# Kernel optimization log

Measured on AMD Instinct MI355X. Metric: run time of the kernel, lower is better.

Reference implementation:

```python
import jax, jax.numpy as jnp
import numpy as np

J = 1.0        # adhesion coupling
TEMP = 1.0     # Metropolis temperature
MCS_STEPS = 4  # monte-carlo sweeps per forward
N_CELL_TYPES = 16


def setup_inputs() -> dict:
    key = jax.random.key(0)
    k1, k2, k3, k4 = jax.random.split(key, 4)
    B, C, H, W = 8, 8, 1024, 1024
    X = jax.random.normal(k1, (B, C, H, W), dtype=jnp.float32)
    # channel 0 is the cell-ID image: small non-negative integer labels
    ids = jax.random.randint(k2, (B, H, W), 0, N_CELL_TYPES).astype(jnp.float32)
    X = X.at[:, 0].set(ids)
    conv_w = jax.random.normal(k3, (4, C), dtype=jnp.float32) * 0.1  # 1x1 conv: C -> 4
    conv_b = jax.random.normal(k4, (4,), dtype=jnp.float32) * 0.1
    return {"X": X, "conv_w": conv_w, "conv_b": conv_b}


def _neighbors(ids):
    # (B,H,W) -> (B,H,W,4): up, down, left, right via periodic roll
    return jnp.stack([
        jnp.roll(ids, (-1, 0), (-2, -1)),
        jnp.roll(ids, (1, 0), (-2, -1)),
        jnp.roll(ids, (0, -1), (-2, -1)),
        jnp.roll(ids, (0, 1), (-2, -1)),
    ], axis=-1)


def _cpm_forward(X, conv_w, conv_b):
    B, C, H, W = X.shape
    # 1x1 conv producing per-direction NN energy term dH_NN: (B,H,W,4)
    dH_NN = jnp.einsum('bchw,oc->bhwo', X, conv_w) + conv_b
    ids = X[:, 0]
    yy = jnp.arange(H)[:, None]
    xx = jnp.arange(W)[None, :]
    parity = ((yy + xx) % 2).astype(jnp.int32)  # checkerboard decomposition

    keys = jax.random.split(jax.random.key(42), 2 * MCS_STEPS)
    subs = jnp.tile(jnp.array([0, 1], jnp.int32), MCS_STEPS)

    def half_step(ids, carry):
        k, sub = carry
        k1, k2 = jax.random.split(k)
        dirs = jax.random.randint(k1, (B, H, W), 0, 4)            # random flip-source direction
        nb = _neighbors(ids)                                       # (B,H,W,4)
        src = jnp.take_along_axis(nb, dirs[..., None], -1)[..., 0]
        # local adhesion dH: J * (unlike-neighbor count after flip - before)
        dH_adh = J * (jnp.sum(nb != src[..., None], -1)
                      - jnp.sum(nb != ids[..., None], -1)).astype(ids.dtype)
        dH_nn = jnp.take_along_axis(dH_NN, dirs[..., None], -1)[..., 0]
        dH = dH_adh + dH_nn
        u = jax.random.uniform(k2, (B, H, W))
        accept = (u < jnp.exp(-dH / TEMP)) & (parity == sub)
        return jnp.where(accept, src, ids), None

    ids, _ = jax.lax.scan(half_step, ids, (keys, subs))
    return X.at[:, 0].set(ids)


def reference(X, conv_w, conv_b):
    return _cpm_forward(X, conv_w, conv_b)
```

## Files before the change

### kernel.cpp

```cpp
#include <hip/hip_runtime.h>
#include <stdint.h>


#define HW    1048576
#define BHWu  8388608u
#define NHu   4194304u

struct KeysK { uint32_t d[8][2]; uint32_t u[8][2]; };

__device__ __host__ __forceinline__ void tf2x32(uint32_t k0, uint32_t k1,
                                                uint32_t x0, uint32_t x1,
                                                uint32_t& o0, uint32_t& o1) {
  uint32_t k2 = k0 ^ k1 ^ 0x1BD11BDAu;
  x0 += k0; x1 += k1;
#define RDD(r) { x0 += x1; x1 = (x1 << (r)) | (x1 >> (32 - (r))); x1 ^= x0; }
  RDD(13) RDD(15) RDD(26) RDD(6)
  x0 += k1; x1 += k2 + 1u;
  RDD(17) RDD(29) RDD(16) RDD(24)
  x0 += k2; x1 += k0 + 2u;
  RDD(13) RDD(15) RDD(26) RDD(6)
  x0 += k0; x1 += k1 + 3u;
  RDD(17) RDD(29) RDD(16) RDD(24)
  x0 += k1; x1 += k2 + 4u;
  RDD(13) RDD(15) RDD(26) RDD(6)
  x0 += k2; x1 += k0 + 5u;
#undef RDD
  o0 = x0; o1 = x1;
}

__device__ __forceinline__ float xla_expf(float input) {
  float x  = fmaxf(fminf(input, 88.3762626647950f), -88.3762626647949f);
  float fx = floorf(fmaf(x, 1.44269504088896341f, 0.5f));
  float tmp = __fmul_rn(0.693359375f, fx);
  float z   = __fmul_rn(-2.12194440e-4f, fx);
  x = __fsub_rn(x, tmp);
  x = __fsub_rn(x, z);
  z = __fmul_rn(x, x);
  float y = fmaf(x, 1.9875691500e-4f, 1.3981999507e-3f);
  y = fmaf(y, x, 8.3334519073e-3f);
  y = fmaf(y, x, 4.1665795894e-2f);
  y = fmaf(y, x, 1.6666665459e-1f);
  y = fmaf(y, x, 5.0000001201e-1f);
  y = fmaf(y, z, x);
  y = __fadd_rn(y, 1.0f);
  int n = (int)fx;
  float p2n = __int_as_float((n + 127) << 23);
  return fmaxf(__fmul_rn(y, p2n), input);
}

#define BY(v, i) ((uint32_t)(((v) >> ((i) * 8)) & 0xffu))
#define ACC_D(dd) (u < xla_expf(-__fadd_rn((float)(dd), v)))

__global__ __launch_bounds__(256) void prep_fused4(const float* __restrict__ X,
                                                   const float* __restrict__ W,
                                                   const float* __restrict__ Bb,
                                                   uint8_t* __restrict__ code,
                                                   uint8_t* __restrict__ ids,
                                                   float* __restrict__ out,
                                                   KeysK K) {
  const uint32_t tid = threadIdx.x;
  const uint32_t g = blockIdx.x, group = g / 23u, r = g - group * 23u;
  if (r >= 16u) {
    uint32_t j = group * 7u + (r - 16u);
    const float4* X4 = (const float4*)X;
    float4*       O4 = (float4*)out;
#pragma unroll
    for (uint32_t i = 0; i < 16u; i++) {
      uint32_t F = j * 4096u + i * 256u + tid;
      uint32_t b = F / 1835008u;
      uint32_t rem = F - b * 1835008u;
      size_t idx = ((size_t)b << 21) + 262144u + rem;
      O4[idx] = X4[idx];
    }
    return;
  }
  const uint32_t row = group * 16u + r;
  const uint32_t b = row >> 10, y = row & 1023u;
  const uint32_t ylsb = y & 1u;
  const uint32_t x0 = 4u * tid;

  const float4* xb = (const float4*)(X + ((size_t)b << 23));
  const uint32_t fq = (y << 8) + tid;

  float acc[4][4];
  float c0[4];
#pragma unroll
  for (int c = 0; c < 8; c++) {
    float4 a = xb[((uint32_t)c << 18) + fq];
    float xs[4] = {a.x, a.y, a.z, a.w};
    if (c == 0) {
#pragma unroll
      for (int px = 0; px < 4; px++) c0[px] = xs[px];
    }
#pragma unroll
    for (int px = 0; px < 4; px++)
#pragma unroll
      for (int o = 0; o < 4; o++) {
        float m = __fmul_rn(xs[px], W[o * 8 + c]);
        acc[px][o] = (c == 0) ? __fadd_rn(0.0f, m) : __fadd_rn(acc[px][o], m);
      }
  }
#pragma unroll
  for (int px = 0; px < 4; px++)
#pragma unroll
    for (int o = 0; o < 4; o++) acc[px][o] = __fadd_rn(acc[px][o], Bb[o]);

  {
    uchar4 v;
    v.x = (uint8_t)(int)c0[0]; v.y = (uint8_t)(int)c0[1];
    v.z = (uint8_t)(int)c0[2]; v.w = (uint8_t)(int)c0[3];
    *(uchar4*)(ids + (b << 20) + (y << 10) + x0) = v;
  }

  const uint32_t pbase   = (b << 20) | (y << 10);
  const uint32_t codeoff = (b << 19) | (y << 9) | (x0 >> 1);
#pragma unroll
  for (int js = 0; js < 4; js++) {
#pragma unroll
    for (int pb = 0; pb < 2; pb++) {
      uint32_t s0 = ylsb ^ (uint32_t)pb;
      uint32_t dka = s0 ? K.d[2 * js + 1][0] : K.d[2 * js][0];
      uint32_t dkb = s0 ? K.d[2 * js + 1][1] : K.d[2 * js][1];
      uint32_t uka = s0 ? K.u[2 * js + 1][0] : K.u[2 * js][0];
      uint32_t ukb = s0 ? K.u[2 * js + 1][1] : K.u[2 * js][1];
      uint32_t cword = 0;
#pragma unroll
      for (int k = 0; k < 2; k++) {
        int px = 2 * k + pb;
        uint32_t p = pbase | (x0 + (uint32_t)px);
        uint32_t o0, o1, q0, q1;
        tf2x32(dka, dkb, 0u, p, o0, o1);
        uint32_t dir = (o0 ^ o1) & 3u;
        tf2x32(uka, ukb, 0u, p, q0, q1);
        uint32_t ub = (q0 ^ q1) >> 9;
        float u = __fsub_rn(__uint_as_float(ub | 0x3F800000u), 1.0f);
        float v = (dir == 0) ? acc[px][0] : (dir == 1) ? acc[px][1]
                : (dir == 2) ? acc[px][2] : acc[px][3];
        int dstar;
        if (ub == 0u) {
          dstar = 4;
        } else {
          float l2  = __log2f(u);
          float tau = fmaf(-0.693147180559945f, l2, -v);
          float gf  = floorf(tau);
          float fr  = tau - gf;
          int   gi  = (int)fmaxf(fminf(gf, 6.0f), -7.0f);
          dstar = gi;
          if (fr < 1e-4f)        dstar = ACC_D(gi)     ? gi     : gi - 1;
          else if (fr > 0.9999f) dstar = ACC_D(gi + 1) ? gi + 1 : gi;
        }
        dstar = dstar < -5 ? -5 : (dstar > 4 ? 4 : dstar);
        cword |= (uint32_t)((uint32_t)(dstar + 5) | (dir << 4)) << (8 * k);
      }
      uint32_t t = 2u * (uint32_t)js + s0;
      *(uint16_t*)(code + (size_t)t * NHu + codeoff) = (uint16_t)cword;
    }
  }
}

template <int LAST>
__global__ __launch_bounds__(256) void step_d(uint8_t* __restrict__ ids,
                                              const uint8_t* __restrict__ codeT,
                                              float* __restrict__ out,
                                              int subi) {
  uint32_t n   = blockIdx.x * 256u + (uint32_t)threadIdx.x;
  uint32_t sub = (uint32_t)subi;
  uint32_t b   = n >> 17;
  uint32_t y   = (n >> 7) & 1023u;
  uint32_t c   = (y + sub) & 1u;
  uint32_t X8  = (n & 127u) << 3;
  uint32_t rowp = (b << 20) | (y << 10);
  uint32_t upp  = (b << 20) | (((y + 1u) & 1023u) << 10);
  uint32_t dnp  = (b << 20) | (((y - 1u) & 1023u) << 10);

  uint32_t cw = *(const uint32_t*)(codeT + ((b << 19) | (y << 9) | ((n & 127u) << 2)));

  uint64_t mid = *(const uint64_t*)(ids + rowp + X8);
  uint64_t up  = *(const uint64_t*)(ids + upp + X8);
  uint64_t dn  = *(const uint64_t*)(ids + dnp + X8);
  uint32_t e   = c ? (uint32_t)ids[rowp + ((X8 + 8u) & 1023u)]
                   : (uint32_t)ids[rowp + ((X8 + 1023u) & 1023u)];

  uint32_t nw[4];
#pragma unroll
  for (int k = 0; k < 4; k++) {
    uint32_t self  = c ? BY(mid, 2 * k + 1) : BY(mid, 2 * k);
    uint32_t left  = c ? BY(mid, 2 * k)
                       : ((k == 0) ? e : BY(mid, 2 * k - 1));
    uint32_t right = c ? ((k == 3) ? e : BY(mid, 2 * k + 2))
                       : BY(mid, 2 * k + 1);
    uint32_t n0 = c ? BY(up, 2 * k + 1) : BY(up, 2 * k);
    uint32_t n1 = c ? BY(dn, 2 * k + 1) : BY(dn, 2 * k);

    uint32_t bk  = (cw >> (8 * k)) & 0xffu;
    uint32_t dir = (bk >> 4) & 3u;
    uint32_t ds5 = bk & 15u;
    uint32_t s  = (dir == 0) ? n0 : (dir == 1) ? n1 : (dir == 2) ? right : left;
    int dadh = ((int)(n0 != s) + (int)(n1 != s) + (int)(right != s) + (int)(left != s))
             - ((int)(n0 != self) + (int)(n1 != self) + (int)(right != self) + (int)(left != self));
    nw[k] = ((uint32_t)(dadh + 5) <= ds5) ? s : self;
  }

  if (!LAST) {
    uint64_t A = (uint64_t)nw[0] | ((uint64_t)nw[1] << 16)
               | ((uint64_t)nw[2] << 32) | ((uint64_t)nw[3] << 48);
    uint64_t mask = 0x00FF00FF00FF00FFull << (8u * c);
    uint64_t nm = (mid & ~mask) | (A << (8u * c));
    *(uint64_t*)(ids + rowp + X8) = nm;
  } else {
    float f[8];
#pragma unroll
    for (int j = 0; j < 8; j++) {
      uint32_t bj = (((uint32_t)j & 1u) == c) ? nw[j >> 1] : BY(mid, j);
      f[j] = (float)bj;
    }
    float4 f0 = {f[0], f[1], f[2], f[3]};
    float4 f1 = {f[4], f[5], f[6], f[7]};
    float* op = out + ((size_t)b << 23) + (y << 10) + X8;
    *(float4*)op       = f0;
    *(float4*)(op + 4) = f1;
  }
}

__device__ __forceinline__ void metro_one(uint32_t u, uint32_t sub,
                                          uint8_t* __restrict__ ids,
                                          const float* __restrict__ dHNN,
                                          uint32_t dk0, uint32_t dk1,
                                          uint32_t uk0, uint32_t uk1) {
  uint32_t b = u >> 19;
  uint32_t r = u & 524287u;
  uint32_t y = r >> 9;
  uint32_t i = r & 511u;
  uint32_t x = (i << 1) | ((y + sub) & 1u);
  uint32_t p = (b << 20) | (y << 10) | x;
  float4 dnn = ((const float4*)dHNN)[sub * NHu + u];
  uint32_t d0, d1, u0, u1;
  tf2x32(dk0, dk1, 0u, p, d0, d1);
  uint32_t db = d0 ^ d1;
  tf2x32(uk0, uk1, 0u, p, u0, u1);
  uint32_t ub = u0 ^ u1;
  int   dir = (int)(db & 3u);
  float uu  = __fsub_rn(__uint_as_float((ub >> 9) | 0x3F800000u), 1.0f);
  uint32_t yN = (y + 1) & 1023u, yP = (y - 1) & 1023u;
  uint32_t xN = (x + 1) & 1023u, xP = (x - 1) & 1023u;
  uint32_t base = b << 20;
  uint32_t cc = ids[p];
  uint32_t n0 = ids[base + (yN << 10) + x];
  uint32_t n1 = ids[base + (yP << 10) + x];
  uint32_t n2 = ids[base + (y << 10) + xN];
  uint32_t n3 = ids[base + (y << 10) + xP];
  uint32_t s  = (dir == 0) ? n0 : (dir == 1) ? n1 : (dir == 2) ? n2 : n3;
  float dH_nn = (dir == 0) ? dnn.x : (dir == 1) ? dnn.y : (dir == 2) ? dnn.z : dnn.w;
  int dadh = ((int)(n0 != s) + (int)(n1 != s) + (int)(n2 != s) + (int)(n3 != s))
           - ((int)(n0 != cc) + (int)(n1 != cc) + (int)(n2 != cc) + (int)(n3 != cc));
  float dH = __fadd_rn((float)dadh, dH_nn);
  if (uu < xla_expf(-dH)) ids[p] = (uint8_t)s;
}

__global__ __launch_bounds__(256) void prep4_fb(const float* __restrict__ X,
                                                const float* __restrict__ W,
                                                const float* __restrict__ Bb,
                                                float* __restrict__ dHNN,
                                                uint8_t* __restrict__ ids) {
  int tid = blockIdx.x * 256 + threadIdx.x;
  int e   = tid << 2;
  int b   = e >> 20;
  int yx  = e & (HW - 1);
  int y   = yx >> 10;
  int x0  = yx & 1023;
  int q4  = yx >> 2;
  const float4* xb = (const float4*)(X + ((size_t)b << 23));
  float4 xc[8];
#pragma unroll
  for (int c = 0; c < 8; c++) xc[c] = xb[(c << 18) + q4];
#pragma unroll
  for (int j = 0; j < 4; j++) {
    float4 r;
#pragma unroll
    for (int o = 0; o < 4; o++) {
      float acc = 0.0f;
#pragma unroll
      for (int c = 0; c < 8; c++)
        acc = __fadd_rn(acc, __fmul_rn(((const float*)&xc[c])[j], W[o * 8 + c]));
      ((float*)&r)[o] = __fadd_rn(acc, Bb[o]);
    }
    int xj = x0 + j;
    ((float4*)dHNN)[((xj + y) & 1) * NHu + (uint32_t)((b << 19) | (y << 9) | (xj >> 1))] = r;
  }
  uchar4 v;
  v.x = (uint8_t)(int)xc[0].x; v.y = (uint8_t)(int)xc[0].y;
  v.z = (uint8_t)(int)xc[0].z; v.w = (uint8_t)(int)xc[0].w;
  *(uchar4*)(ids + e) = v;
}

__global__ __launch_bounds__(256) void half_step_fb(uint8_t* __restrict__ ids,
                                                    const float* __restrict__ dHNN,
                                                    uint32_t dk0, uint32_t dk1,
                                                    uint32_t uk0, uint32_t uk1,
                                                    int sub) {
  uint32_t u = blockIdx.x * 256u + threadIdx.x;
  metro_one(u, (uint32_t)sub, ids, dHNN, dk0, dk1, uk0, uk1);
}

__global__ __launch_bounds__(256) void finalize_full_fb(const float* __restrict__ X,
                                                        const uint8_t* __restrict__ ids,
                                                        float* __restrict__ out) {
  int t = blockIdx.x * 256 + threadIdx.x;
  int e = t << 2;
  int c = (e >> 20) & 7;
  float4 r;
  if (c == 0) {
    int b  = e >> 23;
    int yx = e & (HW - 1);
    uchar4 v = *(const uchar4*)(ids + ((size_t)b << 20) + yx);
    r.x = (float)v.x; r.y = (float)v.y; r.z = (float)v.z; r.w = (float)v.w;
  } else {
    r = ((const float4*)X)[t];
  }
  ((float4*)out)[t] = r;
}

extern "C" void kernel_launch(void* const* d_in, const int* in_sizes, int n_in,
                              void* d_out, int out_size, void* d_ws, size_t ws_size,
                              hipStream_t stream) {
  const float* X  = (const float*)d_in[0];
  const float* W  = (const float*)d_in[1];
  const float* Bb = (const float*)d_in[2];
  float* out = (float*)d_out;

  const size_t CODE_BYTES = (size_t)NHu * 8u;
  const size_t IDS_BYTES  = (size_t)BHWu;

  uint32_t bk0 = 0u, bk1 = 42u;
  uint32_t keys[8][2];
  for (uint32_t t = 0; t < 8; t++)
    tf2x32(bk0, bk1, 0u, t, keys[t][0], keys[t][1]);
  uint32_t K[8][4];
  KeysK KK;
  for (int t = 0; t < 8; t++) {
    uint32_t k1a, k1b;
    tf2x32(keys[t][0], keys[t][1], 0u, 0u, k1a, k1b);
    tf2x32(keys[t][0], keys[t][1], 0u, 1u, K[t][2], K[t][3]);
    tf2x32(k1a, k1b, 0u, 1u, K[t][0], K[t][1]);
    KK.d[t][0] = K[t][0]; KK.d[t][1] = K[t][1];
    KK.u[t][0] = K[t][2]; KK.u[t][1] = K[t][3];
  }

  bool ws_ok = ws_size >= CODE_BYTES + IDS_BYTES;
  if (ws_ok) {
    uint8_t* code = (uint8_t*)d_ws;
    uint8_t* ids  = (uint8_t*)d_ws + CODE_BYTES;

    prep_fused4<<<11776, 256, 0, stream>>>(X, W, Bb, code, ids, out, KK);
    for (int t = 0; t < 7; t++)
      step_d<0><<<4096, 256, 0, stream>>>(ids, code + (size_t)t * NHu, out, t & 1);
    step_d<1><<<4096, 256, 0, stream>>>(ids, code + (size_t)7 * NHu, out, 1);
  } else {
    float*   dHNN = out;
    uint8_t* ids  = (uint8_t*)d_ws;
    prep4_fb<<<8192, 256, 0, stream>>>(X, W, Bb, dHNN, ids);
    for (int t = 0; t < 8; t++)
      half_step_fb<<<16384, 256, 0, stream>>>(ids, dHNN,
          K[t][0], K[t][1], K[t][2], K[t][3], t & 1);
    finalize_full_fb<<<65536, 256, 0, stream>>>(X, ids, out);
  }
  (void)in_sizes; (void)n_in; (void)out_size;
}
```

Before: 238.0 us.

## Fuse pairs of checkerboard half-steps into one ping-pong kernel

Replaces the eight in-place half-step launches with four kernels, each applying two consecutive checkerboard half-steps. The first sub-lattice update is recomputed redundantly for the neighbor rows and edge pixel, and the result goes to a second ids buffer, double-buffered between launches. This halves launch count and global passes over the ids image, at the cost of extra loads and recomputation per thread and doubled ids workspace. The Threefry rotate also switches to the alignbit intrinsic.

Measured after the change: 229.1 us. -3.8%, faster.

```diff
diff --git a/kernel.cpp b/kernel.cpp
--- a/kernel.cpp
+++ b/kernel.cpp
@@ -7,13 +7,19 @@
 #define NHu   4194304u
 
 struct KeysK { uint32_t d[8][2]; uint32_t u[8][2]; };
+
+#ifdef __HIP_DEVICE_COMPILE__
+#define ROTL(v, r) __builtin_amdgcn_alignbit((v), (v), 32u - (r))
+#else
+#define ROTL(v, r) (((v) << (r)) | ((v) >> (32 - (r))))
+#endif
 
 __device__ __host__ __forceinline__ void tf2x32(uint32_t k0, uint32_t k1,
                                                 uint32_t x0, uint32_t x1,
                                                 uint32_t& o0, uint32_t& o1) {
   uint32_t k2 = k0 ^ k1 ^ 0x1BD11BDAu;
   x0 += k0; x1 += k1;
-#define RDD(r) { x0 += x1; x1 = (x1 << (r)) | (x1 >> (32 - (r))); x1 ^= x0; }
+#define RDD(r) { x0 += x1; x1 = ROTL(x1, r) ^ x0; }
   RDD(13) RDD(15) RDD(26) RDD(6)
   x0 += k1; x1 += k2 + 1u;
   RDD(17) RDD(29) RDD(16) RDD(24)
@@ -158,30 +164,19 @@
   }
 }
 
-template <int LAST>
-__global__ __launch_bounds__(256) void step_d(uint8_t* __restrict__ ids,
-                                              const uint8_t* __restrict__ codeT,
-                                              float* __restrict__ out,
-                                              int subi) {
-  uint32_t n   = blockIdx.x * 256u + (uint32_t)threadIdx.x;
-  uint32_t sub = (uint32_t)subi;
-  uint32_t b   = n >> 17;
-  uint32_t y   = (n >> 7) & 1023u;
-  uint32_t c   = (y + sub) & 1u;
-  uint32_t X8  = (n & 127u) << 3;
-  uint32_t rowp = (b << 20) | (y << 10);
-  uint32_t upp  = (b << 20) | (((y + 1u) & 1023u) << 10);
-  uint32_t dnp  = (b << 20) | (((y - 1u) & 1023u) << 10);
-
-  uint32_t cw = *(const uint32_t*)(codeT + ((b << 19) | (y << 9) | ((n & 127u) << 2)));
-
-  uint64_t mid = *(const uint64_t*)(ids + rowp + X8);
-  uint64_t up  = *(const uint64_t*)(ids + upp + X8);
-  uint64_t dn  = *(const uint64_t*)(ids + dnp + X8);
-  uint32_t e   = c ? (uint32_t)ids[rowp + ((X8 + 8u) & 1023u)]
-                   : (uint32_t)ids[rowp + ((X8 + 1023u) & 1023u)];
-
-  uint32_t nw[4];
+__device__ __forceinline__ uint32_t upd1(uint32_t self, uint32_t n0, uint32_t n1,
+                                         uint32_t rt, uint32_t lf, uint32_t bk) {
+  uint32_t dir = (bk >> 4) & 3u;
+  uint32_t ds5 = bk & 15u;
+  uint32_t s = (dir == 0) ? n0 : (dir == 1) ? n1 : (dir == 2) ? rt : lf;
+  int dadh = ((int)(n0 != s) + (int)(n1 != s) + (int)(rt != s) + (int)(lf != s))
+           - ((int)(n0 != self) + (int)(n1 != self) + (int)(rt != self) + (int)(lf != self));
+  return ((uint32_t)(dadh + 5) <= ds5) ? s : self;
+}
+
+__device__ __forceinline__ void upd_row(uint64_t mid, uint64_t up, uint64_t dn,
+                                        uint32_t e, uint32_t c, uint32_t cw,
+                                        uint32_t nw[4]) {
 #pragma unroll
   for (int k = 0; k < 4; k++) {
     uint32_t self  = c ? BY(mid, 2 * k + 1) : BY(mid, 2 * k);
@@ -191,27 +186,87 @@
                        : BY(mid, 2 * k + 1);
     uint32_t n0 = c ? BY(up, 2 * k + 1) : BY(up, 2 * k);
     uint32_t n1 = c ? BY(dn, 2 * k + 1) : BY(dn, 2 * k);
-
-    uint32_t bk  = (cw >> (8 * k)) & 0xffu;
-    uint32_t dir = (bk >> 4) & 3u;
-    uint32_t ds5 = bk & 15u;
-    uint32_t s  = (dir == 0) ? n0 : (dir == 1) ? n1 : (dir == 2) ? right : left;
-    int dadh = ((int)(n0 != s) + (int)(n1 != s) + (int)(right != s) + (int)(left != s))
-             - ((int)(n0 != self) + (int)(n1 != self) + (int)(right != self) + (int)(left != self));
-    nw[k] = ((uint32_t)(dadh + 5) <= ds5) ? s : self;
+    nw[k] = upd1(self, n0, n1, right, left, (cw >> (8 * k)) & 0xffu);
+  }
+}
+
+template <int LAST>
+__global__ __launch_bounds__(256) void step2_d(const uint8_t* __restrict__ in,
+                                               uint8_t* __restrict__ outids,
+                                               const uint8_t* __restrict__ codeA,
+                                               const uint8_t* __restrict__ codeB,
+                                               float* __restrict__ out) {
+  uint32_t n  = blockIdx.x * 256u + (uint32_t)threadIdx.x;
+  uint32_t b  = n >> 17;
+  uint32_t y  = (n >> 7) & 1023u;
+  uint32_t X8 = (n & 127u) << 3;
+  uint32_t base = b << 20;
+  uint32_t ym2 = (y - 2u) & 1023u, ym1 = (y - 1u) & 1023u;
+  uint32_t yp1 = (y + 1u) & 1023u, yp2 = (y + 2u) & 1023u;
+  uint32_t c_a = y & 1u;
+  uint32_t c_b = 1u - c_a;
+
+  uint64_t pm2 = *(const uint64_t*)(in + base + (ym2 << 10) + X8);
+  uint64_t pm1 = *(const uint64_t*)(in + base + (ym1 << 10) + X8);
+  uint64_t p0  = *(const uint64_t*)(in + base + (y   << 10) + X8);
+  uint64_t pp1 = *(const uint64_t*)(in + base + (yp1 << 10) + X8);
+  uint64_t pp2 = *(const uint64_t*)(in + base + (yp2 << 10) + X8);
+
+  uint32_t exL = (X8 + 1023u) & 1023u;
+  uint32_t exR = (X8 + 8u) & 1023u;
+  uint32_t xe  = c_b ? exR : exL;
+  uint32_t yeA = c_a ? exR : exL;
+  uint32_t xo  = c_b ? ((X8 + 9u) & 1023u)
+                     : ((X8 + 1022u) & 1023u);
+
+  uint32_t eA_up = in[base + (yp1 << 10) + xe];
+  uint32_t eA_dn = in[base + (ym1 << 10) + xe];
+  uint32_t eOwn  = in[base + (y << 10) + yeA];
+  uint32_t Eself = in[base + (y << 10) + xe];
+  uint32_t Eout  = in[base + (y << 10) + xo];
+
+  uint32_t cro = (b << 19) | (y   << 9) | (X8 >> 1);
+  uint32_t crm = (b << 19) | (ym1 << 9) | (X8 >> 1);
+  uint32_t crp = (b << 19) | (yp1 << 9) | (X8 >> 1);
+  uint32_t cwA0 = *(const uint32_t*)(codeA + cro);
+  uint32_t cwAm = *(const uint32_t*)(codeA + crm);
+  uint32_t cwAp = *(const uint32_t*)(codeA + crp);
+  uint32_t bkE  = codeA[(b << 19) | (y << 9) | (xe >> 1)];
+  uint32_t cwB  = *(const uint32_t*)(codeB + cro);
+
+  uint32_t nwA0[4], nwAp[4], nwAm[4];
+  upd_row(p0,  pp1, pm1, eOwn,  c_a, cwA0, nwA0);
+  upd_row(pp1, pp2, p0,  eA_up, c_b, cwAp, nwAp);
+  upd_row(pm1, p0,  pm2, eA_dn, c_b, cwAm, nwAm);
+
+  uint32_t Ert, Elf;
+  if (c_b) { Elf = BY(p0, 7); Ert = Eout; }
+  else     { Ert = BY(p0, 0); Elf = Eout; }
+  uint32_t E1 = upd1(Eself, eA_up, eA_dn, Ert, Elf, bkE);
+
+  uint32_t nwB[4];
+#pragma unroll
+  for (int k = 0; k < 4; k++) {
+    uint32_t self = c_b ? BY(p0, 2 * k + 1) : BY(p0, 2 * k);
+    uint32_t lf, rt;
+    if (c_b) { lf = nwA0[k];                 rt = (k == 3) ? E1 : nwA0[k + 1]; }
+    else     { lf = (k == 0) ? E1 : nwA0[k - 1]; rt = nwA0[k]; }
+    nwB[k] = upd1(self, nwAp[k], nwAm[k], rt, lf, (cwB >> (8 * k)) & 0xffu);
   }
 
   if (!LAST) {
-    uint64_t A = (uint64_t)nw[0] | ((uint64_t)nw[1] << 16)
-               | ((uint64_t)nw[2] << 32) | ((uint64_t)nw[3] << 48);
-    uint64_t mask = 0x00FF00FF00FF00FFull << (8u * c);
-    uint64_t nm = (mid & ~mask) | (A << (8u * c));
-    *(uint64_t*)(ids + rowp + X8) = nm;
+    uint64_t A = 0;
+#pragma unroll
+    for (int k = 0; k < 4; k++) {
+      A |= (uint64_t)nwA0[k] << (8 * (2 * k + (int)c_a));
+      A |= (uint64_t)nwB[k]  << (8 * (2 * k + (int)c_b));
+    }
+    *(uint64_t*)(outids + base + (y << 10) + X8) = A;
   } else {
     float f[8];
 #pragma unroll
     for (int j = 0; j < 8; j++) {
-      uint32_t bj = (((uint32_t)j & 1u) == c) ? nw[j >> 1] : BY(mid, j);
+      uint32_t bj = (((uint32_t)j & 1u) == c_a) ? nwA0[j >> 1] : nwB[j >> 1];
       f[j] = (float)bj;
     }
     float4 f0 = {f[0], f[1], f[2], f[3]};
@@ -346,15 +401,21 @@
     KK.u[t][0] = K[t][2]; KK.u[t][1] = K[t][3];
   }
 
-  bool ws_ok = ws_size >= CODE_BYTES + IDS_BYTES;
+  bool ws_ok = ws_size >= CODE_BYTES + 2 * IDS_BYTES;
   if (ws_ok) {
     uint8_t* code = (uint8_t*)d_ws;
-    uint8_t* ids  = (uint8_t*)d_ws + CODE_BYTES;
-
-    prep_fused4<<<11776, 256, 0, stream>>>(X, W, Bb, code, ids, out, KK);
-    for (int t = 0; t < 7; t++)
-      step_d<0><<<4096, 256, 0, stream>>>(ids, code + (size_t)t * NHu, out, t & 1);
-    step_d<1><<<4096, 256, 0, stream>>>(ids, code + (size_t)7 * NHu, out, 1);
+    uint8_t* ids0 = (uint8_t*)d_ws + CODE_BYTES;
+    uint8_t* ids1 = ids0 + IDS_BYTES;
+
+    prep_fused4<<<11776, 256, 0, stream>>>(X, W, Bb, code, ids0, out, KK);
+    step2_d<0><<<4096, 256, 0, stream>>>(ids0, ids1,
+        code + 0 * (size_t)NHu, code + 1 * (size_t)NHu, out);
+    step2_d<0><<<4096, 256, 0, stream>>>(ids1, ids0,
+        code + 2 * (size_t)NHu, code + 3 * (size_t)NHu, out);
+    step2_d<0><<<4096, 256, 0, stream>>>(ids0, ids1,
+        code + 4 * (size_t)NHu, code + 5 * (size_t)NHu, out);
+    step2_d<1><<<4096, 256, 0, stream>>>(ids1, ids0,
+        code + 6 * (size_t)NHu, code + 7 * (size_t)NHu, out);
   } else {
     float*   dHNN = out;
     uint8_t* ids  = (uint8_t*)d_ws;
```
